# Optimization experiments

Hardware: AMD Instinct MI355X
Metric: run time of the kernel (lower is better)

## Reference

```python
import jax, jax.numpy as jnp
import numpy as np

EPS = 1e-3  # keras LayerNormalization / tfa GroupNormalization default epsilon

def _ln(x, g, b):
    m = jnp.mean(x, axis=-1, keepdims=True)
    v = jnp.var(x, axis=-1, keepdims=True)
    return (x - m) / jnp.sqrt(v + EPS) * g + b

def _gn(x, g, b, groups):
    B, D = x.shape
    xg = x.reshape(B, groups, -1)
    m = jnp.mean(xg, axis=-1, keepdims=True)
    v = jnp.var(xg, axis=-1, keepdims=True)
    xn = ((xg - m) / jnp.sqrt(v + EPS)).reshape(B, D)
    return xn * g + b

def _bd(x, w, b):
    # block-diagonal dense: w [H, in/H, out/H], b [out]
    B = x.shape[0]; H = w.shape[0]
    y = jnp.einsum('bhi,hio->bho', x.reshape(B, H, -1), w)
    return y.reshape(B, -1) + b

def setup_inputs() -> dict:
    B, D, HID, NH = 4096, 2048, 2048, 8
    UP = int(HID * 4 / 3)  # 2730
    key = jax.random.key(0)
    ks = jax.random.split(key, 32)
    s = 0.02
    bd_in = lambda k: jax.random.normal(k, (NH, D // NH, HID // NH), jnp.float32) * s
    bd_h = lambda k: jax.random.normal(k, (NH, HID // NH, HID // NH), jnp.float32) * s
    return {
        'x': jax.random.normal(ks[0], (B, D), jnp.float32),
        'h_prev': jax.random.normal(ks[1], (B, HID), jnp.float32),
        'c_prev': jax.random.normal(ks[2], (B, HID), jnp.float32),
        'n_prev': jnp.ones((B, HID), jnp.float32),
        'm_prev': jnp.zeros((B, HID), jnp.float32),
        'ln_g': jnp.ones((D,), jnp.float32), 'ln_b': jnp.zeros((D,), jnp.float32),
        'conv_k': jax.random.normal(ks[3], (4, D, 1), jnp.float32) * s,
        'conv_b': jnp.zeros((1,), jnp.float32),
        'Wz_w': bd_in(ks[4]), 'Wz_b': jnp.zeros((HID,), jnp.float32),
        'Wi_w': bd_in(ks[5]), 'Wi_b': jnp.zeros((HID,), jnp.float32),
        'Wf_w': bd_in(ks[6]), 'Wf_b': jnp.zeros((HID,), jnp.float32),
        'Wo_w': bd_in(ks[7]), 'Wo_b': jnp.zeros((HID,), jnp.float32),
        'Rz_w': bd_h(ks[8]), 'Rz_b': jnp.zeros((HID,), jnp.float32),
        'Ri_w': bd_h(ks[9]), 'Ri_b': jnp.zeros((HID,), jnp.float32),
        'Rf_w': bd_h(ks[10]), 'Rf_b': jnp.zeros((HID,), jnp.float32),
        'Ro_w': bd_h(ks[11]), 'Ro_b': jnp.zeros((HID,), jnp.float32),
        'gn_g': jnp.ones((HID,), jnp.float32), 'gn_b': jnp.zeros((HID,), jnp.float32),
        'upL_w': jax.random.normal(ks[12], (HID, UP), jnp.float32) * s,
        'upL_b': jnp.zeros((UP,), jnp.float32),
        'upR_w': jax.random.normal(ks[13], (HID, UP), jnp.float32) * s,
        'upR_b': jnp.zeros((UP,), jnp.float32),
        'down_w': jax.random.normal(ks[14], (UP, D), jnp.float32) * s,
        'down_b': jnp.zeros((D,), jnp.float32),
    }

def reference(x, h_prev, c_prev, n_prev, m_prev, ln_g, ln_b, conv_k, conv_b,
              Wz_w, Wz_b, Wi_w, Wi_b, Wf_w, Wf_b, Wo_w, Wo_b,
              Rz_w, Rz_b, Ri_w, Ri_b, Rf_w, Rf_b, Ro_w, Ro_b,
              gn_g, gn_b, upL_w, upL_b, upR_w, upR_b, down_w, down_b):
    NH = Wz_w.shape[0]
    x_norm = _ln(x, ln_g, ln_b)
    # CausalConv1D on a length-1 time axis: left zero-pad (k-1) means only the
    # last kernel tap sees x_norm -> scalar per sample; broadcast across channels
    conv_scalar = x_norm @ conv_k[-1, :, 0] + conv_b[0]          # [B]
    x_conv = jnp.broadcast_to(jax.nn.silu(conv_scalar)[:, None], x_norm.shape)
    z = jnp.tanh(_bd(x, Wz_w, Wz_b) + _bd(h_prev, Rz_w, Rz_b))
    o = jax.nn.sigmoid(_bd(x, Wo_w, Wo_b) + _bd(h_prev, Ro_w, Ro_b))
    i_tilde = _bd(x_conv, Wi_w, Wi_b) + _bd(h_prev, Ri_w, Ri_b)
    f_tilde = _bd(x_conv, Wf_w, Wf_b) + _bd(h_prev, Rf_w, Rf_b)
    m_t = jnp.maximum(f_tilde + m_prev, i_tilde)                 # stabilizer
    i = jnp.exp(i_tilde - m_t)
    f = jnp.exp(f_tilde + m_prev - m_t)
    c_t = f * c_prev + i * z
    n_t = f * n_prev + i
    h_t = o * c_t / n_t
    out_norm = _gn(h_t, gn_g, gn_b, NH)
    out_left = out_norm @ upL_w + upL_b
    out_right = out_norm @ upR_w + upR_b
    out = (out_left * jax.nn.gelu(out_right, approximate=False)) @ down_w + down_b
    final_output = out + x
    return (final_output, h_t, c_t, n_t, m_t)
```

## Files before the change

kernel.cpp:

```cpp
#include <hip/hip_runtime.h>
#include <hip/hip_bf16.h>

typedef unsigned short u16;
typedef unsigned int u32x4 __attribute__((ext_vector_type(4)));
typedef __bf16 bf16x8 __attribute__((ext_vector_type(8)));
typedef float f32x4 __attribute__((ext_vector_type(4)));

__device__ __forceinline__ float b2f(u16 u) {
  union { unsigned int i; float f; } v; v.i = ((unsigned int)u) << 16; return v.f;
}
__device__ __forceinline__ u16 f2b(float f) {
  unsigned int x = __builtin_bit_cast(unsigned int, f);
  unsigned int r = (x + 0x7fffu + ((x >> 16) & 1u)) >> 16;
  return (u16)r;
}

__device__ __forceinline__ void stage16(const u16* g, u16* l) {
  __builtin_amdgcn_global_load_lds((const __attribute__((address_space(1))) void*)g,
                                   (__attribute__((address_space(3))) void*)l,
                                   16, 0, 0);
}

__global__ void cvt_k(const float* __restrict__ in, u16* __restrict__ out, long n) {
  long i = ((long)blockIdx.x * 256 + threadIdx.x) * 4;
  if (i + 3 < n) {
    float4 v = *(const float4*)(in + i);
    out[i] = f2b(v.x); out[i+1] = f2b(v.y); out[i+2] = f2b(v.z); out[i+3] = f2b(v.w);
  } else {
    for (long k = i; k < n; ++k) out[k] = f2b(in[k]);
  }
}

__global__ void transpose_k(const float* __restrict__ in, u16* __restrict__ out,
                            int R, int C, int ldo, long ozstride) {
  __shared__ float t[32][33];
  long ibase = (long)blockIdx.z * (long)R * C;
  long obase = (long)blockIdx.z * ozstride;
  int c0 = blockIdx.x * 32, r0 = blockIdx.y * 32;
  for (int i = threadIdx.y; i < 32; i += 8) {
    int r = r0 + i, c = c0 + threadIdx.x;
    t[i][threadIdx.x] = (r < R && c < C) ? in[ibase + (long)r * C + c] : 0.f;
  }
  __syncthreads();
  for (int i = threadIdx.y; i < 32; i += 8) {
    int c = c0 + i, r = r0 + threadIdx.x;
    if (c < C && r < ldo) out[obase + (long)c * ldo + r] = f2b(t[threadIdx.x][i]);
  }
}

__global__ void colsum_k(const float* __restrict__ W, float* __restrict__ out) {
  int h = blockIdx.x, o = threadIdx.x;
  const float* p = W + (long)h * 65536 + o;
  float s = 0.f;
  for (int i = 0; i < 256; ++i) s += p[i * 256];
  out[h * 256 + o] = s;
}

__global__ void ln_conv_k(const float* __restrict__ x, const float* __restrict__ g,
                          const float* __restrict__ bb, const float* __restrict__ ck,
                          const float* __restrict__ cb, float* __restrict__ xc) {
  __shared__ float s1[4], s2[4];
  int b = blockIdx.x, tid = threadIdx.x;
  const float* xr = x + (long)b * 2048;
  float v[8], sum = 0.f, sq = 0.f;
  #pragma unroll
  for (int i = 0; i < 8; ++i) {
    float f = xr[tid + i * 256];
    v[i] = f; sum += f; sq += f * f;
  }
  #pragma unroll
  for (int off = 32; off; off >>= 1) {
    sum += __shfl_down(sum, off, 64);
    sq  += __shfl_down(sq,  off, 64);
  }
  int lane = tid & 63, wv = tid >> 6;
  if (!lane) { s1[wv] = sum; s2[wv] = sq; }
  __syncthreads();
  float tsum = s1[0] + s1[1] + s1[2] + s1[3];
  float tsq  = s2[0] + s2[1] + s2[2] + s2[3];
  float m = tsum * (1.f / 2048.f);
  float var = tsq * (1.f / 2048.f) - m * m;
  float rstd = rsqrtf(var + 1e-3f);
  float dot = 0.f;
  #pragma unroll
  for (int i = 0; i < 8; ++i) {
    int d = tid + i * 256;
    float xn = (v[i] - m) * rstd * g[d] + bb[d];
    dot += xn * ck[3 * 2048 + d];
  }
  #pragma unroll
  for (int off = 32; off; off >>= 1) dot += __shfl_down(dot, off, 64);
  __syncthreads();
  if (!lane) s1[wv] = dot;
  __syncthreads();
  if (tid == 0) {
    float s = s1[0] + s1[1] + s1[2] + s1[3] + cb[0];
    xc[b] = s / (1.f + expf(-s));
  }
}

template<bool F32OUT>
__global__ __launch_bounds__(256) void gemm_bt(
    const u16* __restrict__ A1, long lda1, long sA1,
    const u16* __restrict__ Bt1, long ldb1, long sB1,
    const u16* __restrict__ A2, long lda2, long sA2,
    const u16* __restrict__ Bt2, long ldb2, long sB2,
    int K1, int K2,
    const float* __restrict__ bias,
    const float* __restrict__ res, long ldres,
    void* __restrict__ Cv, long ldc, long sC,
    int M, int N, int nsplit, long off2)
{
  __shared__ u16 As[128][32];
  __shared__ u16 Bs[128][32];
  const int bz = blockIdx.z;
  A1 += (long)bz * sA1; Bt1 += (long)bz * sB1;
  if (A2) { A2 += (long)bz * sA2; Bt2 += (long)bz * sB2; }
  const int m0 = blockIdx.y * 128, n0 = blockIdx.x * 128;
  const int tid = threadIdx.x;
  const int w = tid >> 6, lane = tid & 63;
  const int lr = lane & 15, quad = lane >> 4;
  const int wrow = (w & 1) * 64, wcol = (w >> 1) * 64;
  const int srow = lane >> 2;
  const int scol = (lane & 3) * 8;
  f32x4 acc[4][4] = {};
  const int KT = K1 + K2;
  for (int kk = 0; kk < KT; kk += 32) {
    const u16 *PA, *PB; long lA, lB; int ko;
    if (kk < K1) { PA = A1; lA = lda1; PB = Bt1; lB = ldb1; ko = kk; }
    else         { PA = A2; lA = lda2; PB = Bt2; lB = ldb2; ko = kk - K1; }
    #pragma unroll
    for (int c = 0; c < 2; ++c) {
      const int r0 = (w * 2 + c) * 16;
      long ar = m0 + r0 + srow; if (ar > (long)M - 1) ar = M - 1;
      long br = n0 + r0 + srow; if (br > (long)N - 1) br = N - 1;
      stage16(PA + ar * lA + ko + scol, &As[r0][0]);
      stage16(PB + br * lB + ko + scol, &Bs[r0][0]);
    }
    asm volatile("s_waitcnt vmcnt(0)" ::: "memory");
    __syncthreads();
    bf16x8 af[4], bfr[4];
    #pragma unroll
    for (int i = 0; i < 4; ++i)
      af[i] = __builtin_bit_cast(bf16x8, *(const u32x4*)&As[wrow + i * 16 + lr][quad * 8]);
    #pragma unroll
    for (int j = 0; j < 4; ++j)
      bfr[j] = __builtin_bit_cast(bf16x8, *(const u32x4*)&Bs[wcol + j * 16 + lr][quad * 8]);
    #pragma unroll
    for (int i = 0; i < 4; ++i)
      #pragma unroll
      for (int j = 0; j < 4; ++j)
        acc[i][j] = __builtin_amdgcn_mfma_f32_16x16x32_bf16(af[i], bfr[j], acc[i][j], 0, 0, 0);
    __syncthreads();
  }
  #pragma unroll
  for (int i = 0; i < 4; ++i) {
    #pragma unroll
    for (int r = 0; r < 4; ++r) {
      int row = m0 + wrow + i * 16 + quad * 4 + r;
      if (row >= M) continue;
      #pragma unroll
      for (int j = 0; j < 4; ++j) {
        int col = n0 + wcol + j * 16 + lr;
        if (col >= N) continue;
        float v = acc[i][j][r];
        if (bias) v += bias[col];
        if (res)  v += res[(long)row * ldres + col];
        long e = (long)bz * sC + (long)row * ldc + col;
        if (col >= nsplit) e += off2;
        if (F32OUT) ((float*)Cv)[e] = v;
        else        ((u16*)Cv)[e] = f2b(v);
      }
    }
  }
}

__global__ void gates_k(
    const u16* __restrict__ zpre, const u16* __restrict__ opre,
    const u16* __restrict__ ri,   const u16* __restrict__ rf,
    const float* __restrict__ xc, const float* __restrict__ csi, const float* __restrict__ csf,
    const float* __restrict__ Wz_b, const float* __restrict__ Rz_b,
    const float* __restrict__ Wi_b, const float* __restrict__ Ri_b,
    const float* __restrict__ Wf_b, const float* __restrict__ Rf_b,
    const float* __restrict__ Wo_b, const float* __restrict__ Ro_b,
    const float* __restrict__ c_prev, const float* __restrict__ n_prev, const float* __restrict__ m_prev,
    float* __restrict__ h_out, float* __restrict__ c_out,
    float* __restrict__ n_out, float* __restrict__ m_out)
{
  long idx = (long)blockIdx.x * 256 + threadIdx.x;
  int j = (int)(idx & 2047); long b = idx >> 11;
  float zp = b2f(zpre[idx]) + Wz_b[j] + Rz_b[j];
  float op = b2f(opre[idx]) + Wo_b[j] + Ro_b[j];
  float xcb = xc[b];
  float it = xcb * csi[j] + Wi_b[j] + b2f(ri[idx]) + Ri_b[j];
  float ft = xcb * csf[j] + Wf_b[j] + b2f(rf[idx]) + Rf_b[j];
  float z = tanhf(zp);
  float o = 1.f / (1.f + expf(-op));
  float mp = m_prev[idx];
  float mt = fmaxf(ft + mp, it);
  float ii = expf(it - mt), ff = expf(ft + mp - mt);
  float ct = ff * c_prev[idx] + ii * z;
  float nt = ff * n_prev[idx] + ii;
  float ht = o * ct / nt;
  h_out[idx] = ht; c_out[idx] = ct;
  n_out[idx] = nt; m_out[idx] = mt;
}

__global__ void groupnorm_k(const float* __restrict__ h, const float* __restrict__ gg,
                            const float* __restrict__ gb, u16* __restrict__ onorm) {
  int bg = blockIdx.x; int b = bg >> 3, g = bg & 7;
  long base = (long)b * 2048 + g * 256;
  int lane = threadIdx.x;
  float v[4], sum = 0.f, sq = 0.f;
  #pragma unroll
  for (int i = 0; i < 4; ++i) {
    float f = h[base + lane * 4 + i];
    v[i] = f; sum += f; sq += f * f;
  }
  #pragma unroll
  for (int off = 32; off; off >>= 1) {
    sum += __shfl_down(sum, off, 64);
    sq  += __shfl_down(sq,  off, 64);
  }
  sum = __shfl(sum, 0, 64); sq = __shfl(sq, 0, 64);
  float m = sum * (1.f / 256.f);
  float var = sq * (1.f / 256.f) - m * m;
  float rstd = rsqrtf(var + 1e-3f);
  #pragma unroll
  for (int i = 0; i < 4; ++i) {
    int j = g * 256 + lane * 4 + i;
    onorm[base + lane * 4 + i] = f2b((v[i] - m) * rstd * gg[j] + gb[j]);
  }
}

__global__ void combine_k(u16* __restrict__ buf,
                          const float* __restrict__ lb, const float* __restrict__ rb) {
  int col = blockIdx.x * 256 + threadIdx.x;
  if (col >= 2752) return;
  long base = (long)blockIdx.y * 5504;
  if (col >= 2730) { buf[base + col] = 0; return; }
  float l = b2f(buf[base + col]) + lb[col];
  float r = b2f(buf[base + 2752 + col]) + rb[col];
  float gel = 0.5f * r * (1.f + erff(r * 0.70710678118654752f));
  buf[base + col] = f2b(l * gel);
}

extern "C" void kernel_launch(void* const* d_in, const int* in_sizes, int n_in,
                              void* d_out, int out_size, void* d_ws, size_t ws_size,
                              hipStream_t stream)
{
  const float* x      = (const float*)d_in[0];
  const float* h_prev = (const float*)d_in[1];
  const float* c_prev = (const float*)d_in[2];
  const float* n_prev = (const float*)d_in[3];
  const float* m_prev = (const float*)d_in[4];
  const float* ln_g   = (const float*)d_in[5];
  const float* ln_b   = (const float*)d_in[6];
  const float* conv_k = (const float*)d_in[7];
  const float* conv_b = (const float*)d_in[8];
  const float* Wz_w = (const float*)d_in[9];  const float* Wz_b = (const float*)d_in[10];
  const float* Wi_w = (const float*)d_in[11]; const float* Wi_b = (const float*)d_in[12];
  const float* Wf_w = (const float*)d_in[13]; const float* Wf_b = (const float*)d_in[14];
  const float* Wo_w = (const float*)d_in[15]; const float* Wo_b = (const float*)d_in[16];
  const float* Rz_w = (const float*)d_in[17]; const float* Rz_b = (const float*)d_in[18];
  const float* Ri_w = (const float*)d_in[19]; const float* Ri_b = (const float*)d_in[20];
  const float* Rf_w = (const float*)d_in[21]; const float* Rf_b = (const float*)d_in[22];
  const float* Ro_w = (const float*)d_in[23]; const float* Ro_b = (const float*)d_in[24];
  const float* gn_g = (const float*)d_in[25]; const float* gn_b = (const float*)d_in[26];
  const float* upL_w = (const float*)d_in[27]; const float* upL_b = (const float*)d_in[28];
  const float* upR_w = (const float*)d_in[29]; const float* upR_b = (const float*)d_in[30];
  const float* down_w = (const float*)d_in[31]; const float* down_b = (const float*)d_in[32];

  char* ws = (char*)d_ws;
  u16* zoW   = (u16*)(ws + 0);
  u16* zoR   = (u16*)(ws + 2097152);
  u16* irfW  = (u16*)(ws + 4194304);
  u16* upLT  = (u16*)(ws + 6291456);
  u16* downT = (u16*)(ws + 28655616);
  float* csi = (float*)(ws + 39945216);
  float* csf = (float*)(ws + 39953408);
  float* xc  = (float*)(ws + 39961600);
  u16* zpre  = (u16*)(ws + 39978000 + 2032);
  zpre  = (u16*)(ws + 39980032);
  u16* opre  = (u16*)(ws + 56757248);
  u16* ri    = (u16*)(ws + 73534464);
  u16* rf    = (u16*)(ws + 90311680);
  u16* xb    = (u16*)(ws + 107088896);
  u16* hb    = (u16*)(ws + 123866112);
  u16* onorm = xb;
  u16* updub = zpre;

  float* out   = (float*)d_out;
  float* final_o = out;
  float* hout  = out + 8388608;
  float* cout  = out + 16777216;
  float* nout  = out + 25165824;
  float* mout  = out + 33554432;

  const long GATE_OFF2 = 8388608 - 256;
  const int  NOSPLIT = 1 << 30;

  dim3 tb(32, 8);
  cvt_k<<<8192, 256, 0, stream>>>(x, xb, 8388608);
  cvt_k<<<8192, 256, 0, stream>>>(h_prev, hb, 8388608);
  transpose_k<<<dim3(8, 8, 8), tb, 0, stream>>>(Wz_w, zoW,          256, 256, 256, 131072);
  transpose_k<<<dim3(8, 8, 8), tb, 0, stream>>>(Wo_w, zoW + 65536,  256, 256, 256, 131072);
  transpose_k<<<dim3(8, 8, 8), tb, 0, stream>>>(Rz_w, zoR,          256, 256, 256, 131072);
  transpose_k<<<dim3(8, 8, 8), tb, 0, stream>>>(Ro_w, zoR + 65536,  256, 256, 256, 131072);
  transpose_k<<<dim3(8, 8, 8), tb, 0, stream>>>(Ri_w, irfW,         256, 256, 256, 131072);
  transpose_k<<<dim3(8, 8, 8), tb, 0, stream>>>(Rf_w, irfW + 65536, 256, 256, 256, 131072);
  transpose_k<<<dim3(86, 64, 1), tb, 0, stream>>>(upL_w, upLT, 2048, 2730, 2048, 0);
  transpose_k<<<dim3(86, 64, 1), tb, 0, stream>>>(upR_w, upLT + (long)2730 * 2048, 2048, 2730, 2048, 0);
  transpose_k<<<dim3(64, 86, 1), tb, 0, stream>>>(down_w, downT, 2730, 2048, 2752, 0);
  colsum_k<<<8, 256, 0, stream>>>(Wi_w, csi);
  colsum_k<<<8, 256, 0, stream>>>(Wf_w, csf);
  ln_conv_k<<<4096, 256, 0, stream>>>(x, ln_g, ln_b, conv_k, conv_b, xc);
  gemm_bt<false><<<dim3(4, 32, 8), 256, 0, stream>>>(
      xb, 2048, 256, zoW, 256, 131072, hb, 2048, 256, zoR, 256, 131072,
      256, 256, nullptr, nullptr, 0, zpre, 2048, 256, 4096, 512, 256, GATE_OFF2);
  gemm_bt<false><<<dim3(4, 32, 8), 256, 0, stream>>>(
      hb, 2048, 256, irfW, 256, 131072, nullptr, 0, 0, nullptr, 0, 0,
      256, 0, nullptr, nullptr, 0, ri, 2048, 256, 4096, 512, 256, GATE_OFF2);
  gates_k<<<32768, 256, 0, stream>>>(zpre, opre, ri, rf, xc, csi, csf,
      Wz_b, Rz_b, Wi_b, Ri_b, Wf_b, Rf_b, Wo_b, Ro_b,
      c_prev, n_prev, m_prev, hout, cout, nout, mout);
  groupnorm_k<<<32768, 64, 0, stream>>>(hout, gn_g, gn_b, onorm);
  gemm_bt<false><<<dim3(43, 32, 1), 256, 0, stream>>>(
      onorm, 2048, 0, upLT, 2048, 0, nullptr, 0, 0, nullptr, 0, 0,
      2048, 0, nullptr, nullptr, 0, updub, 5504, 0, 4096, 5460, 2730, 22);
  combine_k<<<dim3(11, 4096), 256, 0, stream>>>(updub, upL_b, upR_b);
  gemm_bt<true><<<dim3(16, 32, 1), 256, 0, stream>>>(
      updub, 5504, 0, downT, 2752, 0, nullptr, 0, 0, nullptr, 0, 0,
      2752, 0, down_b, x, 2048, final_o, 2048, 0, 4096, 2048, NOSPLIT, 0);
}
```

Before: 862.9 us.

## Fuse gates with groupnorm, merge weight transposes, remap GEMM blocks, vectorize elementwise

Several unrelated changes land together. Groupnorm is folded into the gate kernel so h is normalized in registers instead of being re-read, and the x bf16 conversion moves into the layernorm kernel. The six gate-weight transposes, the two up-projection transposes and the two column sums each collapse into one launch, and the column sum is split across more blocks. The GEMM gets an XCD-aware block remapping for better L2 locality, and the gate and combine kernels use 4-wide vector loads and stores. These cut launch count and memory traffic, but the remap and the fused reductions carry some risk.

```diff
diff --git a/kernel.cpp b/kernel.cpp
--- a/kernel.cpp
+++ b/kernel.cpp
@@ -3,6 +3,7 @@
 
 typedef unsigned short u16;
 typedef unsigned int u32x4 __attribute__((ext_vector_type(4)));
+typedef unsigned short us4 __attribute__((ext_vector_type(4)));
 typedef __bf16 bf16x8 __attribute__((ext_vector_type(8)));
 typedef float f32x4 __attribute__((ext_vector_type(4)));
 
@@ -32,41 +33,93 @@
 }
 
 __global__ void transpose_k(const float* __restrict__ in, u16* __restrict__ out,
-                            int R, int C, int ldo, long ozstride) {
+                            int R, int C, int ldo) {
   __shared__ float t[32][33];
-  long ibase = (long)blockIdx.z * (long)R * C;
-  long obase = (long)blockIdx.z * ozstride;
   int c0 = blockIdx.x * 32, r0 = blockIdx.y * 32;
   for (int i = threadIdx.y; i < 32; i += 8) {
     int r = r0 + i, c = c0 + threadIdx.x;
-    t[i][threadIdx.x] = (r < R && c < C) ? in[ibase + (long)r * C + c] : 0.f;
+    t[i][threadIdx.x] = (r < R && c < C) ? in[(long)r * C + c] : 0.f;
   }
   __syncthreads();
   for (int i = threadIdx.y; i < 32; i += 8) {
     int c = c0 + i, r = r0 + threadIdx.x;
-    if (c < C && r < ldo) out[obase + (long)c * ldo + r] = f2b(t[threadIdx.x][i]);
-  }
-}
-
-__global__ void colsum_k(const float* __restrict__ W, float* __restrict__ out) {
-  int h = blockIdx.x, o = threadIdx.x;
-  const float* p = W + (long)h * 65536 + o;
+    if (c < C && r < ldo) out[(long)c * ldo + r] = f2b(t[threadIdx.x][i]);
+  }
+}
+
+__global__ void transpose6_k(const float* __restrict__ Wz, const float* __restrict__ Wo,
+                             const float* __restrict__ Rz, const float* __restrict__ Ro,
+                             const float* __restrict__ Ri, const float* __restrict__ Rf,
+                             u16* __restrict__ zoW, u16* __restrict__ zoR,
+                             u16* __restrict__ irfW) {
+  __shared__ float t[32][33];
+  int zz = blockIdx.z; int wsel = zz >> 3, h = zz & 7;
+  const float* in; u16* outp;
+  switch (wsel) {
+    case 0: in = Wz; outp = zoW;          break;
+    case 1: in = Wo; outp = zoW + 65536;  break;
+    case 2: in = Rz; outp = zoR;          break;
+    case 3: in = Ro; outp = zoR + 65536;  break;
+    case 4: in = Ri; outp = irfW;         break;
+    default: in = Rf; outp = irfW + 65536; break;
+  }
+  in += (long)h * 65536; outp += (long)h * 131072;
+  int c0 = blockIdx.x * 32, r0 = blockIdx.y * 32;
+  for (int i = threadIdx.y; i < 32; i += 8)
+    t[i][threadIdx.x] = in[(long)(r0 + i) * 256 + c0 + threadIdx.x];
+  __syncthreads();
+  for (int i = threadIdx.y; i < 32; i += 8)
+    outp[(long)(c0 + i) * 256 + r0 + threadIdx.x] = f2b(t[threadIdx.x][i]);
+}
+
+__global__ void transpose_up_k(const float* __restrict__ L, const float* __restrict__ R,
+                               u16* __restrict__ out) {
+  __shared__ float t[32][33];
+  const float* in = blockIdx.z ? R : L;
+  u16* o = out + (long)blockIdx.z * 2730 * 2048;
+  int c0 = blockIdx.x * 32, r0 = blockIdx.y * 32;
+  for (int i = threadIdx.y; i < 32; i += 8) {
+    int r = r0 + i, c = c0 + threadIdx.x;
+    t[i][threadIdx.x] = (c < 2730) ? in[(long)r * 2730 + c] : 0.f;
+  }
+  __syncthreads();
+  for (int i = threadIdx.y; i < 32; i += 8) {
+    int c = c0 + i, r = r0 + threadIdx.x;
+    if (c < 2730) o[(long)c * 2048 + r] = f2b(t[threadIdx.x][i]);
+  }
+}
+
+__global__ void colsum2_k(const float* __restrict__ Wi, const float* __restrict__ Wf,
+                          float* __restrict__ csi, float* __restrict__ csf) {
+  const float* W = blockIdx.y ? Wf : Wi;
+  float* outp = blockIdx.y ? csf : csi;
+  int bb = blockIdx.x; int h = bb >> 2, cq = bb & 3;
+  int t = threadIdx.x;
+  int col = cq * 64 + (t & 63);
+  int rg = t >> 6;
+  const float* p = W + (long)h * 65536 + col;
   float s = 0.f;
-  for (int i = 0; i < 256; ++i) s += p[i * 256];
-  out[h * 256 + o] = s;
+  for (int r = rg * 64; r < rg * 64 + 64; ++r) s += p[(long)r * 256];
+  __shared__ float red[4][64];
+  red[rg][t & 63] = s;
+  __syncthreads();
+  if (t < 64) outp[h * 256 + cq * 64 + t] = red[0][t] + red[1][t] + red[2][t] + red[3][t];
 }
 
 __global__ void ln_conv_k(const float* __restrict__ x, const float* __restrict__ g,
                           const float* __restrict__ bb, const float* __restrict__ ck,
-                          const float* __restrict__ cb, float* __restrict__ xc) {
+                          const float* __restrict__ cb, float* __restrict__ xc,
+                          u16* __restrict__ xb) {
   __shared__ float s1[4], s2[4];
   int b = blockIdx.x, tid = threadIdx.x;
   const float* xr = x + (long)b * 2048;
+  u16* xbr = xb + (long)b * 2048;
   float v[8], sum = 0.f, sq = 0.f;
   #pragma unroll
   for (int i = 0; i < 8; ++i) {
     float f = xr[tid + i * 256];
     v[i] = f; sum += f; sq += f * f;
+    xbr[tid + i * 256] = f2b(f);
   }
   #pragma unroll
   for (int off = 32; off; off >>= 1) {
@@ -116,7 +169,14 @@
   const int bz = blockIdx.z;
   A1 += (long)bz * sA1; Bt1 += (long)bz * sB1;
   if (A2) { A2 += (long)bz * sA2; Bt2 += (long)bz * sB2; }
-  const int m0 = blockIdx.y * 128, n0 = blockIdx.x * 128;
+  int gx = gridDim.x;
+  int lin = blockIdx.y * gx + blockIdx.x;
+  int nwg = gx * gridDim.y;
+  if ((nwg & 7) == 0) {
+    int cpx = nwg >> 3;
+    lin = (lin & 7) * cpx + (lin >> 3);
+  }
+  const int m0 = (lin / gx) * 128, n0 = (lin % gx) * 128;
   const int tid = threadIdx.x;
   const int w = tid >> 6, lane = tid & 63;
   const int lr = lane & 15, quad = lane >> 4;
@@ -175,7 +235,7 @@
   }
 }
 
-__global__ void gates_k(
+__global__ void gates_gn_k(
     const u16* __restrict__ zpre, const u16* __restrict__ opre,
     const u16* __restrict__ ri,   const u16* __restrict__ rf,
     const float* __restrict__ xc, const float* __restrict__ csi, const float* __restrict__ csf,
@@ -183,40 +243,48 @@
     const float* __restrict__ Wi_b, const float* __restrict__ Ri_b,
     const float* __restrict__ Wf_b, const float* __restrict__ Rf_b,
     const float* __restrict__ Wo_b, const float* __restrict__ Ro_b,
-    const float* __restrict__ c_prev, const float* __restrict__ n_prev, const float* __restrict__ m_prev,
+    const float* __restrict__ c_prev, const float* __restrict__ n_prev,
+    const float* __restrict__ m_prev,
+    const float* __restrict__ gn_g, const float* __restrict__ gn_b,
     float* __restrict__ h_out, float* __restrict__ c_out,
-    float* __restrict__ n_out, float* __restrict__ m_out)
+    float* __restrict__ n_out, float* __restrict__ m_out,
+    u16* __restrict__ onorm)
 {
-  long idx = (long)blockIdx.x * 256 + threadIdx.x;
-  int j = (int)(idx & 2047); long b = idx >> 11;
-  float zp = b2f(zpre[idx]) + Wz_b[j] + Rz_b[j];
-  float op = b2f(opre[idx]) + Wo_b[j] + Ro_b[j];
+  int t = threadIdx.x;
+  long base = (long)blockIdx.x * 256 + t * 4;
+  int j = (int)(base & 2047);
+  long b = base >> 11;
+  us4 z4 = *(const us4*)(zpre + base);
+  us4 o4 = *(const us4*)(opre + base);
+  us4 i4 = *(const us4*)(ri + base);
+  us4 f4 = *(const us4*)(rf + base);
+  f32x4 cp = *(const f32x4*)(c_prev + base);
+  f32x4 np = *(const f32x4*)(n_prev + base);
+  f32x4 mp = *(const f32x4*)(m_prev + base);
   float xcb = xc[b];
-  float it = xcb * csi[j] + Wi_b[j] + b2f(ri[idx]) + Ri_b[j];
-  float ft = xcb * csf[j] + Wf_b[j] + b2f(rf[idx]) + Rf_b[j];
-  float z = tanhf(zp);
-  float o = 1.f / (1.f + expf(-op));
-  float mp = m_prev[idx];
-  float mt = fmaxf(ft + mp, it);
-  float ii = expf(it - mt), ff = expf(ft + mp - mt);
-  float ct = ff * c_prev[idx] + ii * z;
-  float nt = ff * n_prev[idx] + ii;
-  float ht = o * ct / nt;
-  h_out[idx] = ht; c_out[idx] = ct;
-  n_out[idx] = nt; m_out[idx] = mt;
-}
-
-__global__ void groupnorm_k(const float* __restrict__ h, const float* __restrict__ gg,
-                            const float* __restrict__ gb, u16* __restrict__ onorm) {
-  int bg = blockIdx.x; int b = bg >> 3, g = bg & 7;
-  long base = (long)b * 2048 + g * 256;
-  int lane = threadIdx.x;
-  float v[4], sum = 0.f, sq = 0.f;
-  #pragma unroll
-  for (int i = 0; i < 4; ++i) {
-    float f = h[base + lane * 4 + i];
-    v[i] = f; sum += f; sq += f * f;
-  }
+  float ht[4]; f32x4 ho, co, no, mo;
+  float sum = 0.f, sq = 0.f;
+  #pragma unroll
+  for (int e = 0; e < 4; ++e) {
+    int jj = j + e;
+    float zp = b2f(z4[e]) + Wz_b[jj] + Rz_b[jj];
+    float op = b2f(o4[e]) + Wo_b[jj] + Ro_b[jj];
+    float it = xcb * csi[jj] + Wi_b[jj] + b2f(i4[e]) + Ri_b[jj];
+    float ft = xcb * csf[jj] + Wf_b[jj] + b2f(f4[e]) + Rf_b[jj];
+    float z = tanhf(zp);
+    float o = 1.f / (1.f + expf(-op));
+    float mt = fmaxf(ft + mp[e], it);
+    float ii = expf(it - mt), ff = expf(ft + mp[e] - mt);
+    float ct = ff * cp[e] + ii * z;
+    float nt = ff * np[e] + ii;
+    float h = o * ct / nt;
+    ht[e] = h; ho[e] = h; co[e] = ct; no[e] = nt; mo[e] = mt;
+    sum += h; sq += h * h;
+  }
+  *(f32x4*)(h_out + base) = ho;
+  *(f32x4*)(c_out + base) = co;
+  *(f32x4*)(n_out + base) = no;
+  *(f32x4*)(m_out + base) = mo;
   #pragma unroll
   for (int off = 32; off; off >>= 1) {
     sum += __shfl_down(sum, off, 64);
@@ -226,23 +294,32 @@
   float m = sum * (1.f / 256.f);
   float var = sq * (1.f / 256.f) - m * m;
   float rstd = rsqrtf(var + 1e-3f);
-  #pragma unroll
-  for (int i = 0; i < 4; ++i) {
-    int j = g * 256 + lane * 4 + i;
-    onorm[base + lane * 4 + i] = f2b((v[i] - m) * rstd * gg[j] + gb[j]);
-  }
+  us4 og;
+  #pragma unroll
+  for (int e = 0; e < 4; ++e)
+    og[e] = f2b((ht[e] - m) * rstd * gn_g[j + e] + gn_b[j + e]);
+  *(us4*)(onorm + base) = og;
 }
 
 __global__ void combine_k(u16* __restrict__ buf,
                           const float* __restrict__ lb, const float* __restrict__ rb) {
-  int col = blockIdx.x * 256 + threadIdx.x;
-  if (col >= 2752) return;
-  long base = (long)blockIdx.y * 5504;
-  if (col >= 2730) { buf[base + col] = 0; return; }
-  float l = b2f(buf[base + col]) + lb[col];
-  float r = b2f(buf[base + 2752 + col]) + rb[col];
-  float gel = 0.5f * r * (1.f + erff(r * 0.70710678118654752f));
-  buf[base + col] = f2b(l * gel);
+  int i4 = blockIdx.x * 256 + threadIdx.x;
+  if (i4 >= 688) return;
+  int col = i4 * 4;
+  long base = (long)blockIdx.y * 5504 + col;
+  us4 l4 = *(const us4*)(buf + base);
+  us4 r4 = *(const us4*)(buf + base + 2752);
+  us4 a;
+  #pragma unroll
+  for (int e = 0; e < 4; ++e) {
+    int c = col + e;
+    if (c >= 2730) { a[e] = 0; continue; }
+    float l = b2f(l4[e]) + lb[c];
+    float r = b2f(r4[e]) + rb[c];
+    float gel = 0.5f * r * (1.f + erff(r * 0.70710678118654752f));
+    a[e] = f2b(l * gel);
+  }
+  *(us4*)(buf + base) = a;
 }
 
 extern "C" void kernel_launch(void* const* d_in, const int* in_sizes, int n_in,
@@ -280,8 +357,7 @@
   float* csi = (float*)(ws + 39945216);
   float* csf = (float*)(ws + 39953408);
   float* xc  = (float*)(ws + 39961600);
-  u16* zpre  = (u16*)(ws + 39978000 + 2032);
-  zpre  = (u16*)(ws + 39980032);
+  u16* zpre  = (u16*)(ws + 39980032);
   u16* opre  = (u16*)(ws + 56757248);
   u16* ri    = (u16*)(ws + 73534464);
   u16* rf    = (u16*)(ws + 90311680);
@@ -301,34 +377,26 @@
   const int  NOSPLIT = 1 << 30;
 
   dim3 tb(32, 8);
-  cvt_k<<<8192, 256, 0, stream>>>(x, xb, 8388608);
   cvt_k<<<8192, 256, 0, stream>>>(h_prev, hb, 8388608);
-  transpose_k<<<dim3(8, 8, 8), tb, 0, stream>>>(Wz_w, zoW,          256, 256, 256, 131072);
-  transpose_k<<<dim3(8, 8, 8), tb, 0, stream>>>(Wo_w, zoW + 65536,  256, 256, 256, 131072);
-  transpose_k<<<dim3(8, 8, 8), tb, 0, stream>>>(Rz_w, zoR,          256, 256, 256, 131072);
-  transpose_k<<<dim3(8, 8, 8), tb, 0, stream>>>(Ro_w, zoR + 65536,  256, 256, 256, 131072);
-  transpose_k<<<dim3(8, 8, 8), tb, 0, stream>>>(Ri_w, irfW,         256, 256, 256, 131072);
-  transpose_k<<<dim3(8, 8, 8), tb, 0, stream>>>(Rf_w, irfW + 65536, 256, 256, 256, 131072);
-  transpose_k<<<dim3(86, 64, 1), tb, 0, stream>>>(upL_w, upLT, 2048, 2730, 2048, 0);
-  transpose_k<<<dim3(86, 64, 1), tb, 0, stream>>>(upR_w, upLT + (long)2730 * 2048, 2048, 2730, 2048, 0);
-  transpose_k<<<dim3(64, 86, 1), tb, 0, stream>>>(down_w, downT, 2730, 2048, 2752, 0);
-  colsum_k<<<8, 256, 0, stream>>>(Wi_w, csi);
-  colsum_k<<<8, 256, 0, stream>>>(Wf_w, csf);
-  ln_conv_k<<<4096, 256, 0, stream>>>(x, ln_g, ln_b, conv_k, conv_b, xc);
+  ln_conv_k<<<4096, 256, 0, stream>>>(x, ln_g, ln_b, conv_k, conv_b, xc, xb);
+  transpose6_k<<<dim3(8, 8, 48), tb, 0, stream>>>(Wz_w, Wo_w, Rz_w, Ro_w, Ri_w, Rf_w,
+                                                  zoW, zoR, irfW);
+  transpose_up_k<<<dim3(86, 64, 2), tb, 0, stream>>>(upL_w, upR_w, upLT);
+  transpose_k<<<dim3(64, 86, 1), tb, 0, stream>>>(down_w, downT, 2730, 2048, 2752);
+  colsum2_k<<<dim3(32, 2), 256, 0, stream>>>(Wi_w, Wf_w, csi, csf);
   gemm_bt<false><<<dim3(4, 32, 8), 256, 0, stream>>>(
       xb, 2048, 256, zoW, 256, 131072, hb, 2048, 256, zoR, 256, 131072,
       256, 256, nullptr, nullptr, 0, zpre, 2048, 256, 4096, 512, 256, GATE_OFF2);
   gemm_bt<false><<<dim3(4, 32, 8), 256, 0, stream>>>(
       hb, 2048, 256, irfW, 256, 131072, nullptr, 0, 0, nullptr, 0, 0,
       256, 0, nullptr, nullptr, 0, ri, 2048, 256, 4096, 512, 256, GATE_OFF2);
-  gates_k<<<32768, 256, 0, stream>>>(zpre, opre, ri, rf, xc, csi, csf,
+  gates_gn_k<<<32768, 64, 0, stream>>>(zpre, opre, ri, rf, xc, csi, csf,
       Wz_b, Rz_b, Wi_b, Ri_b, Wf_b, Rf_b, Wo_b, Ro_b,
-      c_prev, n_prev, m_prev, hout, cout, nout, mout);
-  groupnorm_k<<<32768, 64, 0, stream>>>(hout, gn_g, gn_b, onorm);
+      c_prev, n_prev, m_prev, gn_g, gn_b, hout, cout, nout, mout, onorm);
   gemm_bt<false><<<dim3(43, 32, 1), 256, 0, stream>>>(
       onorm, 2048, 0, upLT, 2048, 0, nullptr, 0, 0, nullptr, 0, 0,
       2048, 0, nullptr, nullptr, 0, updub, 5504, 0, 4096, 5460, 2730, 22);
-  combine_k<<<dim3(11, 4096), 256, 0, stream>>>(updub, upL_b, upR_b);
+  combine_k<<<dim3(3, 4096), 256, 0, stream>>>(updub, upL_b, upR_b);
   gemm_bt<true><<<dim3(16, 32, 1), 256, 0, stream>>>(
       updub, 5504, 0, downT, 2752, 0, nullptr, 0, 0, nullptr, 0, 0,
       2752, 0, down_b, x, 2048, final_o, 2048, 0, 4096, 2048, NOSPLIT, 0);
```

Result: no change. 869.8 us (+0.8%).
